# Optimization experiments

Hardware: AMD Instinct MI355X
Metric: run time of the kernel (lower is better)

## Reference

```python
import jax, jax.numpy as jnp
import numpy as np

VOCAB = 2_000_000
NUM_TAGS = 32
SEQ_LEN = 16384
START = 0  # tag2id['<s>']
END = 1    # tag2id['</s>']


def setup_inputs() -> dict:
    key = jax.random.key(0)
    k1, k2, k3 = jax.random.split(key, 3)
    x = jax.random.randint(k1, (SEQ_LEN,), 0, VOCAB)
    emit_score = jax.random.normal(k2, (VOCAB, NUM_TAGS), dtype=jnp.float32)
    transitions = jax.random.normal(k3, (NUM_TAGS, NUM_TAGS), dtype=jnp.float32)
    # same masking as the torch __init__
    transitions = transitions.at[:, START].set(-10000.0)
    transitions = transitions.at[END, :].set(-10000.0)
    return {"x": x, "emit_score": emit_score, "transitions": transitions}


def reference(x, emit_score, transitions):
    """CRF forward algorithm (log partition function Z), fused via lax.scan."""
    num_tags = transitions.shape[0]
    init_alphas = jnp.full((num_tags,), -10000.0, dtype=transitions.dtype)
    init_alphas = init_alphas.at[START].set(0.0)

    emits = emit_score[x]  # [L, T] gather (memory-bound)

    def step(alphas, emit_t):
        # score[i, j] = alphas[i] + transitions[i, j] + emit_t[j]
        score = alphas[:, None] + transitions + emit_t[None, :]
        new_alphas = jax.nn.logsumexp(score, axis=0)  # stable log-sum-exp over prev tag
        return new_alphas, None

    alphas, _ = jax.lax.scan(step, init_alphas, emits)
    alphas = alphas + transitions[:, END]
    z = jax.nn.logsumexp(alphas)  # scalar log partition
    return z
```

## Files before the change

kernel.cpp:

```cpp
#include <hip/hip_runtime.h>

#define LOG2E 1.44269504088896340736f
#define LN2   0.69314718055994530942f

static constexpr int NT     = 32;
static constexpr int SEQ    = 16384;
static constexpr int LC     = 64;
static constexpr int CHUNKS = SEQ / LC;
static constexpr int GROUP  = 16;
static constexpr int NB2    = CHUNKS / GROUP;

typedef __attribute__((ext_vector_type(8)))  short short8;
typedef __attribute__((ext_vector_type(16))) float float16_t;

union U8 { unsigned u[4]; short8 s; };

__device__ __forceinline__ unsigned pack_bf16(float a, float b) {
    unsigned ua = (__float_as_uint(a) + 0x8000u) >> 16;
    unsigned ub = (__float_as_uint(b) + 0x8000u) & 0xFFFF0000u;
    return ua | ub;
}

__device__ __forceinline__ float wave_max(float v) {
    #pragma unroll
    for (int m = 1; m <= 32; m <<= 1) v = fmaxf(v, __shfl_xor(v, m, 64));
    return v;
}

#define PACK_SWAP_TO_B(ACC, B0, B1)                                          \
    {                                                                        \
        unsigned P0 = pack_bf16(ACC[0],  ACC[1]);                            \
        unsigned P1 = pack_bf16(ACC[2],  ACC[3]);                            \
        unsigned P2 = pack_bf16(ACC[4],  ACC[5]);                            \
        unsigned P3 = pack_bf16(ACC[6],  ACC[7]);                            \
        unsigned P4 = pack_bf16(ACC[8],  ACC[9]);                            \
        unsigned P5 = pack_bf16(ACC[10], ACC[11]);                           \
        unsigned P6 = pack_bf16(ACC[12], ACC[13]);                           \
        unsigned P7 = pack_bf16(ACC[14], ACC[15]);                           \
        unsigned q0 = __shfl_xor(P0, 32, 64), q1 = __shfl_xor(P1, 32, 64);   \
        unsigned q2 = __shfl_xor(P2, 32, 64), q3 = __shfl_xor(P3, 32, 64);   \
        unsigned q4 = __shfl_xor(P4, 32, 64), q5 = __shfl_xor(P5, 32, 64);   \
        unsigned q6 = __shfl_xor(P6, 32, 64), q7 = __shfl_xor(P7, 32, 64);   \
        B0.u[0] = hi ? q2 : P0; B0.u[1] = hi ? q3 : P1;                      \
        B0.u[2] = hi ? P2 : q0; B0.u[3] = hi ? P3 : q1;                      \
        B1.u[0] = hi ? q6 : P4; B1.u[1] = hi ? q7 : P5;                      \
        B1.u[2] = hi ? P6 : q4; B1.u[3] = hi ? P7 : q5;                      \
    }

#define IDENTITY_B(B0, B1)                                                   \
    {                                                                        \
        _Pragma("unroll")                                                    \
        for (int q = 0; q < 4; ++q) {                                        \
            unsigned lo = ((8*h + 2*q)     == c) ? 0x3F80u : 0u;             \
            unsigned hb = ((8*h + 2*q + 1) == c) ? 0x3F80u : 0u;             \
            B0.u[q] = lo | (hb << 16);                                       \
            lo = ((16 + 8*h + 2*q)     == c) ? 0x3F80u : 0u;                 \
            hb = ((16 + 8*h + 2*q + 1) == c) ? 0x3F80u : 0u;                 \
            B1.u[q] = lo | (hb << 16);                                       \
        }                                                                    \
    }

__global__ __launch_bounds__(64, 1)
void crf_phase1(const int* __restrict__ x, const float* __restrict__ emit,
                const float* __restrict__ trans,
                float* __restrict__ out1, float* __restrict__ out1S)
{
    __shared__ __align__(16) float E[LC * NT];
    const int L = threadIdx.x;
    const int c = L & 31;
    const int h = L >> 5;
    const bool hi = (h != 0);
    const int chunk = blockIdx.x;

    int xv = x[chunk * LC + L];
    float ev[32];
    #pragma unroll
    for (int rr = 0; rr < 32; ++rr) {
        int t = 2 * rr + h;
        int xt = __shfl(xv, t, 64);
        ev[rr] = emit[(size_t)xt * NT + c];
    }
    #pragma unroll
    for (int rr = 0; rr < 32; ++rr) {
        int t = 2 * rr + h;
        E[t * NT + c] = exp2f(ev[rr] * LOG2E);
    }
    __syncthreads();

    U8 A0, A1;
    #pragma unroll
    for (int q = 0; q < 4; ++q) {
        float w0 = exp2f(trans[(8*h + 2*q    ) * NT + c] * LOG2E);
        float w1 = exp2f(trans[(8*h + 2*q + 1) * NT + c] * LOG2E);
        A0.u[q] = pack_bf16(w0, w1);
        float w2 = exp2f(trans[(16 + 8*h + 2*q    ) * NT + c] * LOG2E);
        float w3 = exp2f(trans[(16 + 8*h + 2*q + 1) * NT + c] * LOG2E);
        A1.u[q] = pack_bf16(w2, w3);
    }

    U8 B0, B1;
    IDENTITY_B(B0, B1);

    int sInt = 0;
    float16_t acc;
    for (int t = 0; t < LC; ++t) {
        float16_t z = {};
        acc = __builtin_amdgcn_mfma_f32_32x32x16_bf16(A0.s, B0.s, z,   0, 0, 0);
        acc = __builtin_amdgcn_mfma_f32_32x32x16_bf16(A1.s, B1.s, acc, 0, 0, 0);

        const float* Et = &E[t * NT + 4 * h];
        float4 e0 = *(const float4*)(Et);
        float4 e1 = *(const float4*)(Et + 8);
        float4 e2 = *(const float4*)(Et + 16);
        float4 e3 = *(const float4*)(Et + 24);
        acc[0]  *= e0.x; acc[1]  *= e0.y; acc[2]  *= e0.z; acc[3]  *= e0.w;
        acc[4]  *= e1.x; acc[5]  *= e1.y; acc[6]  *= e1.z; acc[7]  *= e1.w;
        acc[8]  *= e2.x; acc[9]  *= e2.y; acc[10] *= e2.z; acc[11] *= e2.w;
        acc[12] *= e3.x; acc[13] *= e3.y; acc[14] *= e3.z; acc[15] *= e3.w;

        if ((t & 3) == 3) {
            float mx = acc[0];
            #pragma unroll
            for (int i = 1; i < 16; ++i) mx = fmaxf(mx, acc[i]);
            mx = wave_max(mx);
            if (mx >= 1.1754944e-38f) {
                int ex = (int)((__float_as_uint(mx) >> 23) & 255) - 127;
                #pragma unroll
                for (int i = 0; i < 16; ++i) acc[i] = ldexpf(acc[i], -ex);
                sInt += ex;
            }
        }
        PACK_SWAP_TO_B(acc, B0, B1);
    }

    float mx = acc[0];
    #pragma unroll
    for (int i = 1; i < 16; ++i) mx = fmaxf(mx, acc[i]);
    mx = wave_max(mx);
    float lm = log2f(mx);
    float* o = out1 + (size_t)chunk * (NT * NT);
    #pragma unroll
    for (int i = 0; i < 16; ++i) {
        int r = 4 * h + (i & 3) + 8 * (i >> 2);
        o[r * NT + c] = log2f(acc[i]) - lm;
    }
    if (L == 0) out1S[chunk] = (float)sInt + lm;
}

__global__ __launch_bounds__(64, 1)
void crf_phase2a(const float* __restrict__ out1, const float* __restrict__ out1S,
                 float* __restrict__ out2)
{
    const int L = threadIdx.x;
    const int c = L & 31;
    const int h = L >> 5;
    const bool hi = (h != 0);
    const int w = blockIdx.x;

    U8 B0, B1;
    IDENTITY_B(B0, B1);

    float SC = 0.f;
    #pragma unroll
    for (int n = 0; n < GROUP; ++n) SC += out1S[w * GROUP + n];

    const float* src = out1 + (size_t)(w * GROUP) * (NT * NT) + c * NT + 8 * h;
    float4 a0 = *(const float4*)(src);
    float4 a1 = *(const float4*)(src + 4);
    float4 a2 = *(const float4*)(src + 16);
    float4 a3 = *(const float4*)(src + 20);

    int sInt = 0;
    float16_t acc;
    for (int n = 0; n < GROUP; ++n) {
        U8 A0, A1;
        A0.u[0] = pack_bf16(exp2f(a0.x), exp2f(a0.y));
        A0.u[1] = pack_bf16(exp2f(a0.z), exp2f(a0.w));
        A0.u[2] = pack_bf16(exp2f(a1.x), exp2f(a1.y));
        A0.u[3] = pack_bf16(exp2f(a1.z), exp2f(a1.w));
        A1.u[0] = pack_bf16(exp2f(a2.x), exp2f(a2.y));
        A1.u[1] = pack_bf16(exp2f(a2.z), exp2f(a2.w));
        A1.u[2] = pack_bf16(exp2f(a3.x), exp2f(a3.y));
        A1.u[3] = pack_bf16(exp2f(a3.z), exp2f(a3.w));

        if (n + 1 < GROUP) {
            const float* s2 = out1 + (size_t)(w * GROUP + n + 1) * (NT * NT)
                              + c * NT + 8 * h;
            a0 = *(const float4*)(s2);
            a1 = *(const float4*)(s2 + 4);
            a2 = *(const float4*)(s2 + 16);
            a3 = *(const float4*)(s2 + 20);
        }

        float16_t z = {};
        acc = __builtin_amdgcn_mfma_f32_32x32x16_bf16(A0.s, B0.s, z,   0, 0, 0);
        acc = __builtin_amdgcn_mfma_f32_32x32x16_bf16(A1.s, B1.s, acc, 0, 0, 0);

        float mx = acc[0];
        #pragma unroll
        for (int i = 1; i < 16; ++i) mx = fmaxf(mx, acc[i]);
        mx = wave_max(mx);
        if (mx >= 1.1754944e-38f) {
            int ex = (int)((__float_as_uint(mx) >> 23) & 255) - 127;
            #pragma unroll
            for (int i = 0; i < 16; ++i) acc[i] = ldexpf(acc[i], -ex);
            sInt += ex;
        }
        PACK_SWAP_TO_B(acc, B0, B1);
    }

    float* o = out2 + (size_t)w * (NT * NT);
    float addc = (float)sInt + SC;
    #pragma unroll
    for (int i = 0; i < 16; ++i) {
        int r = 4 * h + (i & 3) + 8 * (i >> 2);
        o[r * NT + c] = log2f(acc[i]) + addc;
    }
}

__global__ __launch_bounds__(64, 1)
void crf_phase2b(const float* __restrict__ out2, const float* __restrict__ trans,
                 float* __restrict__ out)
{
    __shared__ __align__(16) float al[NT];
    const int L = threadIdx.x;
    const int r = L & 31;
    const int h = L >> 5;

    if (L < NT) al[L] = (L == 0) ? 0.f : -10000.f * LOG2E;
    __syncthreads();

    const float* src = out2 + r * NT + 16 * h;
    float4 v0 = *(const float4*)(src);
    float4 v1 = *(const float4*)(src + 4);
    float4 v2 = *(const float4*)(src + 8);
    float4 v3 = *(const float4*)(src + 12);

    for (int n = 0; n < NB2; ++n) {
        float vals[16] = {v0.x, v0.y, v0.z, v0.w, v1.x, v1.y, v1.z, v1.w,
                          v2.x, v2.y, v2.z, v2.w, v3.x, v3.y, v3.z, v3.w};
        if (n + 1 < NB2) {
            const float* s2 = out2 + (size_t)(n + 1) * (NT * NT) + r * NT + 16 * h;
            v0 = *(const float4*)(s2);
            v1 = *(const float4*)(s2 + 4);
            v2 = *(const float4*)(s2 + 8);
            v3 = *(const float4*)(s2 + 12);
        }
        const float4* ap = (const float4*)&al[16 * h];
        float4 A0 = ap[0], A1 = ap[1], A2 = ap[2], A3 = ap[3];
        float aj[16] = {A0.x, A0.y, A0.z, A0.w, A1.x, A1.y, A1.z, A1.w,
                        A2.x, A2.y, A2.z, A2.w, A3.x, A3.y, A3.z, A3.w};
        float mv = -3.0e38f;
        #pragma unroll
        for (int j = 0; j < 16; ++j) {
            vals[j] = fmaxf(vals[j], -1e30f) + fmaxf(aj[j], -1e30f);
            mv = fmaxf(mv, vals[j]);
        }
        mv = fmaxf(mv, __shfl_xor(mv, 32, 64));
        float s = 0.f;
        #pragma unroll
        for (int j = 0; j < 16; ++j) s += exp2f(vals[j] - mv);
        s += __shfl_xor(s, 32, 64);
        float nal = mv + log2f(s);
        __syncthreads();
        if (h == 0) al[r] = nal;
        __syncthreads();
    }

    float v = fmaxf(al[r], -1e30f) + trans[r * NT + 1] * LOG2E;
    float mv = v;
    #pragma unroll
    for (int m = 1; m <= 16; m <<= 1) mv = fmaxf(mv, __shfl_xor(mv, m, 64));
    float s = exp2f(v - mv);
    #pragma unroll
    for (int m = 1; m <= 16; m <<= 1) s += __shfl_xor(s, m, 64);
    if (L == 0) out[0] = (mv + log2f(s)) * LN2;
}

extern "C" void kernel_launch(void* const* d_in, const int* in_sizes, int n_in,
                              void* d_out, int out_size, void* d_ws, size_t ws_size,
                              hipStream_t stream) {
    const int*   x     = (const int*)d_in[0];
    const float* emit  = (const float*)d_in[1];
    const float* trans = (const float*)d_in[2];
    float* out = (float*)d_out;

    float* ws1   = (float*)d_ws;
    float* ws2   = ws1 + (size_t)CHUNKS * NT * NT;
    float* ws1S  = ws2 + (size_t)NB2 * NT * NT;

    crf_phase1 <<<CHUNKS, 64, 0, stream>>>(x, emit, trans, ws1, ws1S);
    crf_phase2a<<<NB2,    64, 0, stream>>>(ws1, ws1S, ws2);
    crf_phase2b<<<1,      64, 0, stream>>>(ws2, trans, out);
}
```

Baseline: 328.1 us.

## Halve CRF chunk length and pass chunk matrices between phases as bf16

Shortens phase-1 chunks from 64 to 32 steps, which doubles the number of parallel chunk blocks and halves each block's serial MFMA chain. It also adds phase-2a work, since NB2 doubles. Phase 1 now writes bf16 linear-domain matrices with an integer exponent offset instead of fp32 log values, so phase 2a can feed them straight into the MFMA operands without exp2/pack. Phase 2b keeps the alpha vector in registers and broadcasts it with shuffles, removing shared memory and two barriers per step. Precision may drop slightly from storing bf16 and skipping the final max-normalisation.

```diff
diff --git a/kernel.cpp b/kernel.cpp
--- a/kernel.cpp
+++ b/kernel.cpp
@@ -5,7 +5,7 @@
 
 static constexpr int NT     = 32;
 static constexpr int SEQ    = 16384;
-static constexpr int LC     = 64;
+static constexpr int LC     = 32;
 static constexpr int CHUNKS = SEQ / LC;
 static constexpr int GROUP  = 16;
 static constexpr int NB2    = CHUNKS / GROUP;
@@ -60,10 +60,24 @@
         }                                                                    \
     }
 
+#define MATRIX_RESCALE(ACC, SINT)                                            \
+    {                                                                        \
+        float mx = ACC[0];                                                   \
+        _Pragma("unroll")                                                    \
+        for (int i = 1; i < 16; ++i) mx = fmaxf(mx, ACC[i]);                 \
+        mx = wave_max(mx);                                                   \
+        if (mx >= 1.1754944e-38f) {                                          \
+            int ex = (int)((__float_as_uint(mx) >> 23) & 255) - 127;         \
+            _Pragma("unroll")                                                \
+            for (int i = 0; i < 16; ++i) ACC[i] = ldexpf(ACC[i], -ex);       \
+            SINT += ex;                                                      \
+        }                                                                    \
+    }
+
 __global__ __launch_bounds__(64, 1)
 void crf_phase1(const int* __restrict__ x, const float* __restrict__ emit,
                 const float* __restrict__ trans,
-                float* __restrict__ out1, float* __restrict__ out1S)
+                unsigned short* __restrict__ out1b, float* __restrict__ out1S)
 {
     __shared__ __align__(16) float E[LC * NT];
     const int L = threadIdx.x;
@@ -72,19 +86,17 @@
     const bool hi = (h != 0);
     const int chunk = blockIdx.x;
 
-    int xv = x[chunk * LC + L];
-    float ev[32];
-    #pragma unroll
-    for (int rr = 0; rr < 32; ++rr) {
+    int xv = x[chunk * LC + c];
+    float ev[16];
+    #pragma unroll
+    for (int rr = 0; rr < 16; ++rr) {
         int t = 2 * rr + h;
         int xt = __shfl(xv, t, 64);
         ev[rr] = emit[(size_t)xt * NT + c];
     }
     #pragma unroll
-    for (int rr = 0; rr < 32; ++rr) {
-        int t = 2 * rr + h;
-        E[t * NT + c] = exp2f(ev[rr] * LOG2E);
-    }
+    for (int rr = 0; rr < 16; ++rr)
+        E[(2 * rr + h) * NT + c] = exp2f(ev[rr] * LOG2E);
     __syncthreads();
 
     U8 A0, A1;
@@ -118,38 +130,22 @@
         acc[8]  *= e2.x; acc[9]  *= e2.y; acc[10] *= e2.z; acc[11] *= e2.w;
         acc[12] *= e3.x; acc[13] *= e3.y; acc[14] *= e3.z; acc[15] *= e3.w;
 
-        if ((t & 3) == 3) {
-            float mx = acc[0];
-            #pragma unroll
-            for (int i = 1; i < 16; ++i) mx = fmaxf(mx, acc[i]);
-            mx = wave_max(mx);
-            if (mx >= 1.1754944e-38f) {
-                int ex = (int)((__float_as_uint(mx) >> 23) & 255) - 127;
-                #pragma unroll
-                for (int i = 0; i < 16; ++i) acc[i] = ldexpf(acc[i], -ex);
-                sInt += ex;
-            }
-        }
-        PACK_SWAP_TO_B(acc, B0, B1);
-    }
-
-    float mx = acc[0];
-    #pragma unroll
-    for (int i = 1; i < 16; ++i) mx = fmaxf(mx, acc[i]);
-    mx = wave_max(mx);
-    float lm = log2f(mx);
-    float* o = out1 + (size_t)chunk * (NT * NT);
+        if ((t & 3) == 3) MATRIX_RESCALE(acc, sInt);
+        if (t + 1 < LC) PACK_SWAP_TO_B(acc, B0, B1);
+    }
+
+    unsigned short* o = out1b + (size_t)chunk * (NT * NT);
     #pragma unroll
     for (int i = 0; i < 16; ++i) {
         int r = 4 * h + (i & 3) + 8 * (i >> 2);
-        o[r * NT + c] = log2f(acc[i]) - lm;
-    }
-    if (L == 0) out1S[chunk] = (float)sInt + lm;
+        o[r * NT + c] = (unsigned short)((__float_as_uint(acc[i]) + 0x8000u) >> 16);
+    }
+    if (L == 0) out1S[chunk] = (float)sInt;
 }
 
 __global__ __launch_bounds__(64, 1)
-void crf_phase2a(const float* __restrict__ out1, const float* __restrict__ out1S,
-                 float* __restrict__ out2)
+void crf_phase2a(const unsigned short* __restrict__ out1b,
+                 const float* __restrict__ out1S, float* __restrict__ out2)
 {
     const int L = threadIdx.x;
     const int c = L & 31;
@@ -164,49 +160,30 @@
     #pragma unroll
     for (int n = 0; n < GROUP; ++n) SC += out1S[w * GROUP + n];
 
-    const float* src = out1 + (size_t)(w * GROUP) * (NT * NT) + c * NT + 8 * h;
-    float4 a0 = *(const float4*)(src);
-    float4 a1 = *(const float4*)(src + 4);
-    float4 a2 = *(const float4*)(src + 16);
-    float4 a3 = *(const float4*)(src + 20);
+    const unsigned* src = (const unsigned*)(out1b + (size_t)(w * GROUP) * (NT * NT));
+    uint4 a0 = *(const uint4*)(src + c * 16 + 4 * h);
+    uint4 a1 = *(const uint4*)(src + c * 16 + 8 + 4 * h);
 
     int sInt = 0;
     float16_t acc;
     for (int n = 0; n < GROUP; ++n) {
         U8 A0, A1;
-        A0.u[0] = pack_bf16(exp2f(a0.x), exp2f(a0.y));
-        A0.u[1] = pack_bf16(exp2f(a0.z), exp2f(a0.w));
-        A0.u[2] = pack_bf16(exp2f(a1.x), exp2f(a1.y));
-        A0.u[3] = pack_bf16(exp2f(a1.z), exp2f(a1.w));
-        A1.u[0] = pack_bf16(exp2f(a2.x), exp2f(a2.y));
-        A1.u[1] = pack_bf16(exp2f(a2.z), exp2f(a2.w));
-        A1.u[2] = pack_bf16(exp2f(a3.x), exp2f(a3.y));
-        A1.u[3] = pack_bf16(exp2f(a3.z), exp2f(a3.w));
+        A0.u[0] = a0.x; A0.u[1] = a0.y; A0.u[2] = a0.z; A0.u[3] = a0.w;
+        A1.u[0] = a1.x; A1.u[1] = a1.y; A1.u[2] = a1.z; A1.u[3] = a1.w;
 
         if (n + 1 < GROUP) {
-            const float* s2 = out1 + (size_t)(w * GROUP + n + 1) * (NT * NT)
-                              + c * NT + 8 * h;
-            a0 = *(const float4*)(s2);
-            a1 = *(const float4*)(s2 + 4);
-            a2 = *(const float4*)(s2 + 16);
-            a3 = *(const float4*)(s2 + 20);
+            const unsigned* s2 = (const unsigned*)
+                (out1b + (size_t)(w * GROUP + n + 1) * (NT * NT));
+            a0 = *(const uint4*)(s2 + c * 16 + 4 * h);
+            a1 = *(const uint4*)(s2 + c * 16 + 8 + 4 * h);
         }
 
         float16_t z = {};
         acc = __builtin_amdgcn_mfma_f32_32x32x16_bf16(A0.s, B0.s, z,   0, 0, 0);
         acc = __builtin_amdgcn_mfma_f32_32x32x16_bf16(A1.s, B1.s, acc, 0, 0, 0);
 
-        float mx = acc[0];
-        #pragma unroll
-        for (int i = 1; i < 16; ++i) mx = fmaxf(mx, acc[i]);
-        mx = wave_max(mx);
-        if (mx >= 1.1754944e-38f) {
-            int ex = (int)((__float_as_uint(mx) >> 23) & 255) - 127;
-            #pragma unroll
-            for (int i = 0; i < 16; ++i) acc[i] = ldexpf(acc[i], -ex);
-            sInt += ex;
-        }
-        PACK_SWAP_TO_B(acc, B0, B1);
+        MATRIX_RESCALE(acc, sInt);
+        if (n + 1 < GROUP) PACK_SWAP_TO_B(acc, B0, B1);
     }
 
     float* o = out2 + (size_t)w * (NT * NT);
@@ -222,13 +199,11 @@
 void crf_phase2b(const float* __restrict__ out2, const float* __restrict__ trans,
                  float* __restrict__ out)
 {
-    __shared__ __align__(16) float al[NT];
     const int L = threadIdx.x;
     const int r = L & 31;
     const int h = L >> 5;
 
-    if (L < NT) al[L] = (L == 0) ? 0.f : -10000.f * LOG2E;
-    __syncthreads();
+    float alr = (r == 0) ? 0.f : -10000.f * LOG2E;
 
     const float* src = out2 + r * NT + 16 * h;
     float4 v0 = *(const float4*)(src);
@@ -246,14 +221,11 @@
             v2 = *(const float4*)(s2 + 8);
             v3 = *(const float4*)(s2 + 12);
         }
-        const float4* ap = (const float4*)&al[16 * h];
-        float4 A0 = ap[0], A1 = ap[1], A2 = ap[2], A3 = ap[3];
-        float aj[16] = {A0.x, A0.y, A0.z, A0.w, A1.x, A1.y, A1.z, A1.w,
-                        A2.x, A2.y, A2.z, A2.w, A3.x, A3.y, A3.z, A3.w};
         float mv = -3.0e38f;
         #pragma unroll
         for (int j = 0; j < 16; ++j) {
-            vals[j] = fmaxf(vals[j], -1e30f) + fmaxf(aj[j], -1e30f);
+            float aj = __shfl(alr, 16 * h + j, 64);
+            vals[j] = fmaxf(vals[j], -1e30f) + fmaxf(aj, -1e30f);
             mv = fmaxf(mv, vals[j]);
         }
         mv = fmaxf(mv, __shfl_xor(mv, 32, 64));
@@ -261,13 +233,10 @@
         #pragma unroll
         for (int j = 0; j < 16; ++j) s += exp2f(vals[j] - mv);
         s += __shfl_xor(s, 32, 64);
-        float nal = mv + log2f(s);
-        __syncthreads();
-        if (h == 0) al[r] = nal;
-        __syncthreads();
-    }
-
-    float v = fmaxf(al[r], -1e30f) + trans[r * NT + 1] * LOG2E;
+        alr = mv + log2f(s);
+    }
+
+    float v = fmaxf(alr, -1e30f) + trans[r * NT + 1] * LOG2E;
     float mv = v;
     #pragma unroll
     for (int m = 1; m <= 16; m <<= 1) mv = fmaxf(mv, __shfl_xor(mv, m, 64));
@@ -285,11 +254,12 @@
     const float* trans = (const float*)d_in[2];
     float* out = (float*)d_out;
 
-    float* ws1   = (float*)d_ws;
-    float* ws2   = ws1 + (size_t)CHUNKS * NT * NT;
-    float* ws1S  = ws2 + (size_t)NB2 * NT * NT;
-
-    crf_phase1 <<<CHUNKS, 64, 0, stream>>>(x, emit, trans, ws1, ws1S);
-    crf_phase2a<<<NB2,    64, 0, stream>>>(ws1, ws1S, ws2);
+    char* ws = (char*)d_ws;
+    unsigned short* ws1b = (unsigned short*)ws;
+    float* ws1S = (float*)(ws + (size_t)CHUNKS * NT * NT * 2);
+    float* ws2  = ws1S + CHUNKS;
+
+    crf_phase1 <<<CHUNKS, 64, 0, stream>>>(x, emit, trans, ws1b, ws1S);
+    crf_phase2a<<<NB2,    64, 0, stream>>>(ws1b, ws1S, ws2);
     crf_phase2b<<<1,      64, 0, stream>>>(ws2, trans, out);
 }
```

New measurement: 332.0 us. Within noise of the previous version (+1.2%).
